# Performance work log

Hardware: AMD Instinct MI355X
Metric: run time of the kernel (lower is better)

Reference implementation:

```python
import jax, jax.numpy as jnp
import numpy as np

DK, DV, NH = 512, 256, 8  # matches init_kwargs


def rel_to_abs(x):
    # x: (B, N, L, 2L-1) -> (B, N, L, L) via pad/reshape trick
    B, N, L, _ = x.shape
    x = jnp.pad(x, ((0, 0), (0, 0), (0, 0), (0, 1)))          # (B,N,L,2L)
    x = x.reshape(B, N, L * 2 * L)
    x = jnp.pad(x, ((0, 0), (0, 0), (0, L - 1)))
    x = x.reshape(B, N, L + 1, 2 * L - 1)
    return x[:, :, :L, L - 1:]


def relative_logits_1d(q, rel_k):
    # q: (B, nh, A, Wd, dkh); rel_k: (dkh, 2*Wd-1)
    B, nh, A, Wd, _ = q.shape
    rel = jnp.einsum('bnawc,cm->bnawm', q, rel_k)             # (B,nh,A,Wd,2Wd-1)
    rel = rel.reshape(B, nh * A, Wd, 2 * Wd - 1)
    rel = rel_to_abs(rel).reshape(B, nh, A, 1, Wd, Wd)
    return jnp.broadcast_to(rel, (B, nh, A, A, Wd, Wd))


def reference(x, w_qkv, w_conv, w_out, key_rel_h, key_rel_w):
    B, Cin, H, W = x.shape
    dkh, dvh = DK // NH, DV // NH
    L = H * W
    # 1x1 qkv projection (stride 1)
    qkv = jnp.einsum('bchw,oc->bohw', x, w_qkv)               # (B, 2dk+dv, H, W)
    q = qkv[:, :DK]
    k = qkv[:, DK:2 * DK]
    v = qkv[:, 2 * DK:]
    flat_q = q.reshape(B, NH, dkh, L) * (dkh ** -0.5)
    flat_k = k.reshape(B, NH, dkh, L)
    flat_v = v.reshape(B, NH, dvh, L)
    logits = jnp.einsum('bncs,bnct->bnst', flat_q, flat_k)     # (B,nh,L,L)
    # relative position logits (uses the already-scaled q, as in the torch code)
    qr = flat_q.reshape(B, NH, dkh, H, W).transpose(0, 1, 3, 4, 2)  # (B,nh,H,W,dkh)
    w_rel = relative_logits_1d(qr, key_rel_w)                  # (B,nh,H,H,W,W)
    h_rel = relative_logits_1d(qr.transpose(0, 1, 3, 2, 4), key_rel_h)  # (B,nh,W,W,H,H)
    h_rel = h_rel.transpose(0, 1, 2, 4, 3, 5).reshape(B, NH, L, L)
    w_rel = w_rel.transpose(0, 1, 4, 2, 5, 3).reshape(B, NH, L, L)
    logits = logits + h_rel + w_rel
    weights = jax.nn.softmax(logits, axis=-1)
    attn = jnp.einsum('bnst,bnct->bnsc', weights, flat_v)      # (B,nh,L,dvh)
    attn = attn.transpose(0, 1, 3, 2).reshape(B, DV, H, W)
    attn = jnp.einsum('bchw,oc->bohw', attn, w_out)            # 1x1 out_proj
    conv_out = jax.lax.conv_general_dilated(
        x, w_conv, window_strides=(1, 1), padding=[(1, 1), (1, 1)],
        dimension_numbers=('NCHW', 'OIHW', 'NCHW'))            # (B, out_c-dv, H, W)
    return jnp.concatenate([conv_out, attn], axis=1)


def setup_inputs() -> dict:
    key = jax.random.key(0)
    ks = jax.random.split(key, 6)
    H, W, Cin = 32, 32, 256
    return {
        'x': jax.random.normal(ks[0], (8, Cin, H, W), jnp.float32),
        'w_qkv': jax.random.normal(ks[1], (2 * DK + DV, Cin), jnp.float32) * 0.02,
        'w_conv': jax.random.normal(ks[2], (256, Cin, 3, 3), jnp.float32) * 0.02,
        'w_out': jax.random.normal(ks[3], (DV, DV), jnp.float32) * 0.02,
        'key_rel_h': DK ** -0.5 + jax.random.normal(ks[4], (DK // NH, 2 * H - 1), jnp.float32),
        'key_rel_w': DK ** -0.5 + jax.random.normal(ks[5], (DK // NH, 2 * W - 1), jnp.float32),
    }
```

## Files before the change

### kernel.cpp

```cpp
#include <hip/hip_runtime.h>
#include <cstddef>
#include <cstdint>

#define NB 8
#define CIN 256
#define LL 1024
#define DKC 512
#define DVC 256
#define XPSTRIDE 295936

typedef short short8 __attribute__((ext_vector_type(8)));
typedef float f32x4 __attribute__((ext_vector_type(4)));

__device__ __forceinline__ unsigned short f2bf(float f) {
  unsigned int u = __float_as_uint(f);
  u += 0x7fffu + ((u >> 16) & 1u);
  return (unsigned short)(u >> 16);
}
__device__ __forceinline__ float bf2f(unsigned short u) {
  return __uint_as_float(((unsigned int)u) << 16);
}

__global__ __launch_bounds__(256) void prep_all(
    const float* __restrict__ x, const float* __restrict__ wconv,
    const float* __restrict__ wqkv, const float* __restrict__ wout,
    const float* __restrict__ krh, const float* __restrict__ krw,
    unsigned short* __restrict__ xTp, unsigned short* __restrict__ wtap,
    unsigned short* __restrict__ wqbf, unsigned short* __restrict__ woutbf,
    unsigned short* __restrict__ relTh, unsigned short* __restrict__ relTw) {
  __shared__ float tile[64][65];
  const int bx = blockIdx.x;
  const int tid = threadIdx.x;
  if (bx < 128) {
    const int st = bx & 15;
    const int b = bx >> 4;
    const int s0 = st * 64;
    const int h0 = st * 2;
    for (int cc = 0; cc < 4; ++cc) {
      const int c0 = cc * 64;
      {
        const int row = tid >> 2;
        const int j0 = (tid & 3) * 16;
#pragma unroll
        for (int k = 0; k < 4; ++k)
          *(float4*)&tile[row][j0 + k * 4] =
              *(const float4*)(x + ((size_t)(b * CIN + c0 + row)) * LL + s0 + j0 + k * 4);
      }
      __syncthreads();
      {
        const int sl = tid >> 2;
        const int cb = (tid & 3) * 16;
        unsigned short buf[16];
#pragma unroll
        for (int m = 0; m < 16; ++m) buf[m] = f2bf(tile[cb + m][sl]);
        const int hp = h0 + (sl >> 5) + 1;
        const int wp = (sl & 31) + 1;
        unsigned short* dst = xTp + (size_t)b * XPSTRIDE + (hp * 34 + wp) * 256 + c0 + cb;
        *(uint4*)dst = *(uint4*)&buf[0];
        *(uint4*)(dst + 8) = *(uint4*)&buf[8];
      }
      __syncthreads();
    }
  } else if (bx < 1184) {
    const int idx = (bx - 128) * 256 + tid;
    const int b = idx / 33792;
    const int rem = idx - b * 33792;
    const int pos = rem >> 8, c = rem & 255;
    int hp, wp;
    if (pos < 34) { hp = 0; wp = pos; }
    else if (pos < 68) { hp = 33; wp = pos - 34; }
    else if (pos < 100) { hp = pos - 68 + 1; wp = 0; }
    else { hp = pos - 100 + 1; wp = 33; }
    xTp[(size_t)b * XPSTRIDE + (hp * 34 + wp) * 256 + c] = 0;
  } else {
    const int idx = (bx - 1184) * 256 + tid;
    if (idx < 589824) {
      const int tap = idx >> 16;
      const int rem = idx & 65535;
      wtap[idx] = f2bf(wconv[(size_t)rem * 9 + tap]);
    } else if (idx < 917504) {
      const int j = idx - 589824;
      const int o = j >> 8;
      const float sc = (o < DKC) ? 0.125f * 1.44269504088896f : 1.0f;
      wqbf[j] = f2bf(wqkv[j] * sc);
    } else if (idx < 983040) {
      const int j = idx - 917504;
      woutbf[j] = f2bf(wout[j]);
    } else {
      const int j = idx - 983040;
      const int tbl = j >> 12;
      const int rest = j & 4095;
      const int m = rest >> 6, c = rest & 63;
      const float* src = tbl ? krw : krh;
      unsigned short* dst = tbl ? relTw : relTh;
      const float v = (m < 63) ? src[c * 63 + m] : 0.f;
      dst[m * 64 + c] = f2bf(v);
    }
  }
}

__global__ __launch_bounds__(256) void qkv_mfma(
    const unsigned short* __restrict__ xTp, const unsigned short* __restrict__ wqbf,
    unsigned short* __restrict__ qbf, unsigned short* __restrict__ kbf,
    unsigned short* __restrict__ vbf) {
  __shared__ __align__(16) char smem[16640];
  unsigned short* as = (unsigned short*)smem;
  unsigned short* bs = (unsigned short*)(smem + 8192);
  float (*trans)[65] = (float(*)[65])smem;

  const int tid = threadIdx.x;
  const int lane = tid & 63, w = tid >> 6;
  const int n16 = lane & 15, quad = lane >> 4;
  const int ot = blockIdx.x;
  const int st = blockIdx.y;
  const int b = blockIdx.z;
  const int o0 = ot * 64;
  const int s0 = st * 64;
  const int h0 = st * 2;
  const int trow = tid >> 3, ck = tid & 7;

  const unsigned short* xb = xTp + (size_t)b * XPSTRIDE;
  const unsigned short* wt = wqbf + (size_t)o0 * 256;
  const int wpos = (trow & 31) + 1;

  f32x4 acc[4];
#pragma unroll
  for (int nt = 0; nt < 4; ++nt) acc[nt] = (f32x4){0.f, 0.f, 0.f, 0.f};

  uint4 ra0, ra1, rb0, rb1;
  {
    ra0 = *(const uint4*)(wt + (size_t)trow * 256 + ck * 8);
    ra1 = *(const uint4*)(wt + (size_t)(trow + 32) * 256 + ck * 8);
    rb0 = *(const uint4*)(xb + (size_t)((h0 + 1) * 34 + wpos) * 256 + ck * 8);
    rb1 = *(const uint4*)(xb + (size_t)((h0 + 2) * 34 + wpos) * 256 + ck * 8);
  }
#pragma unroll
  for (int kc = 0; kc < 4; ++kc) {
    __syncthreads();
    *(uint4*)&as[trow * 64 + ((ck ^ (trow & 7)) * 8)] = ra0;
    *(uint4*)&as[(trow + 32) * 64 + ((ck ^ (trow & 7)) * 8)] = ra1;
    *(uint4*)&bs[trow * 64 + ((ck ^ (trow & 7)) * 8)] = rb0;
    *(uint4*)&bs[(trow + 32) * 64 + ((ck ^ (trow & 7)) * 8)] = rb1;
    __syncthreads();
    if (kc < 3) {
      const int c0 = (kc + 1) * 64;
      ra0 = *(const uint4*)(wt + (size_t)trow * 256 + c0 + ck * 8);
      ra1 = *(const uint4*)(wt + (size_t)(trow + 32) * 256 + c0 + ck * 8);
      rb0 = *(const uint4*)(xb + (size_t)((h0 + 1) * 34 + wpos) * 256 + c0 + ck * 8);
      rb1 = *(const uint4*)(xb + (size_t)((h0 + 2) * 34 + wpos) * 256 + c0 + ck * 8);
    }
    short8 a0 = *(const short8*)&as[(w * 16 + n16) * 64 + ((quad ^ (n16 & 7)) * 8)];
    short8 a1 = *(const short8*)&as[(w * 16 + n16) * 64 + (((quad + 4) ^ (n16 & 7)) * 8)];
#pragma unroll
    for (int nt = 0; nt < 4; ++nt) {
      short8 b0 = *(const short8*)&bs[(nt * 16 + n16) * 64 + ((quad ^ (n16 & 7)) * 8)];
      short8 b1 = *(const short8*)&bs[(nt * 16 + n16) * 64 + (((quad + 4) ^ (n16 & 7)) * 8)];
      acc[nt] = __builtin_amdgcn_mfma_f32_16x16x32_bf16(a0, b0, acc[nt], 0, 0, 0);
      acc[nt] = __builtin_amdgcn_mfma_f32_16x16x32_bf16(a1, b1, acc[nt], 0, 0, 0);
    }
  }
  __syncthreads();
#pragma unroll
  for (int nt = 0; nt < 4; ++nt)
#pragma unroll
    for (int reg = 0; reg < 4; ++reg)
      trans[w * 16 + quad * 4 + reg][nt * 16 + n16] = acc[nt][reg];
  __syncthreads();
  const int sl = tid >> 2;
  const int cseg = (tid & 3) * 16;
  unsigned short buf[16];
  if (ot < 16) {
#pragma unroll
    for (int m = 0; m < 16; ++m) buf[m] = f2bf(trans[cseg + m][sl]);
    unsigned short* dst;
    int head;
    if (ot < 8) { dst = qbf; head = ot; }
    else { dst = kbf; head = ot - 8; }
    const size_t base = (((size_t)(b * 8 + head)) * LL + s0 + sl) * 64 + cseg;
    *(uint4*)(dst + base) = *(uint4*)&buf[0];
    *(uint4*)(dst + base + 8) = *(uint4*)&buf[8];
  } else {
#pragma unroll
    for (int m = 0; m < 16; ++m) buf[m] = f2bf(trans[sl][cseg + m]);
    unsigned short* dst = vbf + ((size_t)b * DVC + (ot - 16) * 64 + sl) * LL + s0 + cseg;
    *(uint4*)dst = *(uint4*)&buf[0];
    *(uint4*)(dst + 8) = *(uint4*)&buf[8];
  }
}

__global__ __launch_bounds__(256, 4) void attn_kernel(
    const unsigned short* __restrict__ qbf, const unsigned short* __restrict__ kbf,
    const unsigned short* __restrict__ vbf, const unsigned short* __restrict__ relTh,
    const unsigned short* __restrict__ relTw, unsigned short* __restrict__ abf) {
  __shared__ __align__(16) char smem[32768];
  unsigned short* ks = (unsigned short*)smem;
  unsigned short* vs = (unsigned short*)(smem + 16384);
  unsigned short* rwtT = (unsigned short*)(smem + 24576);
  unsigned short* ps = (unsigned short*)(smem + 8192);
  float* obuf = (float*)smem;

  const int tid = threadIdx.x;
  const int lane = tid & 63, w = tid >> 6;
  const int n16 = lane & 15, quad = lane >> 4;
  const int blk = blockIdx.x;
  const int bn = blk & 63, qb = blk >> 6;
  const int n = bn & 7, b = bn >> 3;
  const int s0 = qb * 64;
  const int aa = 2 * qb + (w >> 1);
  const int pb = (w & 1) * 16;

  const unsigned short* qbase = qbf + ((size_t)(b * 8 + n)) * LL * 64;
  const unsigned short* kbase = kbf + ((size_t)(b * 8 + n)) * LL * 64;
  const unsigned short* vbase = vbf + ((size_t)(b * 8 + n)) * 32 * LL;

  const int ck = tid & 7;
  const int trow = tid >> 3;
  const int keyt = (trow & 3) | (((trow >> 3) & 1) << 2);
  const int krb = (n16 >> 2) * 8 + (n16 & 3);
  const int kk = (n16 & 3) | (((n16 >> 2) & 1) << 2);
  const int vk = (n16 & 3) | (((n16 >> 3) & 1) << 2);
  const int qcol = w * 16 + n16;

  uint4 pk0 = *(const uint4*)(kbase + trow * 64 + ck * 8);
  uint4 pk1 = *(const uint4*)(kbase + (trow + 32) * 64 + ck * 8);
  uint4 pv = *(const uint4*)(vbase + (size_t)trow * LL + ck * 8);

  {
    const int sT = (pb + n16) * 32 + aa;
    short8 ra0 = *(const short8*)(qbase + (size_t)sT * 64 + quad * 8);
    short8 ra1 = *(const short8*)(qbase + (size_t)sT * 64 + 32 + quad * 8);
#pragma unroll
    for (int tbl = 0; tbl < 2; ++tbl) {
      const unsigned short* rel = tbl ? relTh : relTw;
      f32x4 acc[4];
#pragma unroll
      for (int mt = 0; mt < 4; ++mt) acc[mt] = (f32x4){0.f, 0.f, 0.f, 0.f};
#pragma unroll
      for (int mt = 0; mt < 4; ++mt) {
        short8 b0 = *(const short8*)(rel + (mt * 16 + n16) * 64 + quad * 8);
        short8 b1 = *(const short8*)(rel + (mt * 16 + n16) * 64 + 32 + quad * 8);
        acc[mt] = __builtin_amdgcn_mfma_f32_16x16x32_bf16(ra0, b0, acc[mt], 0, 0, 0);
        acc[mt] = __builtin_amdgcn_mfma_f32_16x16x32_bf16(ra1, b1, acc[mt], 0, 0, 0);
      }
      if (tbl == 0) {
#pragma unroll
        for (int mt = 0; mt < 4; ++mt)
#pragma unroll
          for (int reg = 0; reg < 4; ++reg)
            rwtT[(mt * 16 + n16) * 64 +
                 ((w * 16 + quad * 4 + reg) ^ ((n16 & 7) * 8))] = f2bf(acc[mt][reg]);
      } else {
#pragma unroll
        for (int mt = 0; mt < 4; ++mt)
#pragma unroll
          for (int reg = 0; reg < 4; ++reg)
            ps[(w * 16 + quad * 4 + reg) * 64 + mt * 16 + n16] = f2bf(acc[mt][reg]);
      }
    }
  }
  short8 qf0 = *(const short8*)(qbase + (size_t)(s0 + w * 16 + n16) * 64 + quad * 8);
  short8 qf1 = *(const short8*)(qbase + (size_t)(s0 + w * 16 + n16) * 64 + 32 + quad * 8);
  {
    *(uint4*)&ks[trow * 64 + ((ck ^ keyt) * 8)] = pk0;
    *(uint4*)&ks[(trow + 32) * 64 + ((ck ^ keyt) * 8)] = pk1;
    *(uint4*)&vs[trow * 64 + ((ck ^ keyt) * 8)] = pv;
  }
  __syncthreads();
  float rhreg[2][4];
#pragma unroll
  for (int c1 = 0; c1 < 2; ++c1)
#pragma unroll
    for (int reg = 0; reg < 4; ++reg)
      rhreg[c1][reg] =
          bf2f(ps[qcol * 64 + quad * 8 + c1 * 4 + reg + 31 - pb - n16]);
  __syncthreads();

  float lacc[4] = {0.f, 0.f, 0.f, 0.f};
  f32x4 oacc[2];
  oacc[0] = (f32x4){0.f, 0.f, 0.f, 0.f};
  oacc[1] = (f32x4){0.f, 0.f, 0.f, 0.f};

  int cur = 0;
  for (int kt64 = 0; kt64 < 16; ++kt64) {
    const int t0 = kt64 * 64;
    if (kt64 < 15) {
      const unsigned short* kg = kbase + (size_t)(t0 + 64) * 64;
      pk0 = *(const uint4*)(kg + trow * 64 + ck * 8);
      pk1 = *(const uint4*)(kg + (trow + 32) * 64 + ck * 8);
      pv = *(const uint4*)(vbase + (size_t)trow * LL + t0 + 64 + ck * 8);
    }
    __syncthreads();
    const unsigned short* ksb = ks + cur * 4096;
    const unsigned short* vsb = vs + cur * 2048;

    f32x4 sacc[4];
#pragma unroll
    for (int c = 0; c < 4; ++c) sacc[c] = (f32x4){0.f, 0.f, 0.f, 0.f};
#pragma unroll
    for (int c = 0; c < 4; ++c) {
      const int ro = (krb + (c & 1) * 4 + (c >> 1) * 32) * 64;
      short8 kb0 = *(const short8*)&ksb[ro + ((quad ^ kk) * 8)];
      short8 kb1 = *(const short8*)&ksb[ro + (((quad + 4) ^ kk) * 8)];
      sacc[c] = __builtin_amdgcn_mfma_f32_16x16x32_bf16(kb0, qf0, sacc[c], 0, 0, 0);
      sacc[c] = __builtin_amdgcn_mfma_f32_16x16x32_bf16(kb1, qf1, sacc[c], 0, 0, 0);
    }
    float rww[2];
#pragma unroll
    for (int h = 0; h < 2; ++h) {
      const int mw = (t0 >> 5) + h - aa + 31;
      rww[h] = bf2f(rwtT[mw * 64 + (qcol ^ ((mw & 7) * 8))]);
    }
    unsigned int pkw[2][4];
#pragma unroll
    for (int c = 0; c < 4; ++c) {
      float e[4];
#pragma unroll
      for (int reg = 0; reg < 4; ++reg) {
        e[reg] = __builtin_amdgcn_exp2f(sacc[c][reg] + rww[c >> 1] + rhreg[c & 1][reg]);
        lacc[reg] += e[reg];
      }
      unsigned int p0, p1;
      asm("v_cvt_pk_bf16_f32 %0, %1, %2" : "=v"(p0) : "v"(e[0]), "v"(e[1]));
      asm("v_cvt_pk_bf16_f32 %0, %1, %2" : "=v"(p1) : "v"(e[2]), "v"(e[3]));
      pkw[c >> 1][(c & 1) * 2] = p0;
      pkw[c >> 1][(c & 1) * 2 + 1] = p1;
    }
#pragma unroll
    for (int kt = 0; kt < 2; ++kt) {
      uint4 pw;
      pw.x = pkw[kt][0]; pw.y = pkw[kt][1]; pw.z = pkw[kt][2]; pw.w = pkw[kt][3];
      short8 pa = *(short8*)&pw;
#pragma unroll
      for (int ct = 0; ct < 2; ++ct) {
        short8 vb = *(const short8*)&vsb[(ct * 16 + n16) * 64 + (((quad + 4 * kt) ^ vk) * 8)];
        oacc[ct] = __builtin_amdgcn_mfma_f32_16x16x32_bf16(pa, vb, oacc[ct], 0, 0, 0);
      }
    }
    if (kt64 < 15) {
      unsigned short* kd = ks + (cur ^ 1) * 4096;
      unsigned short* vd = vs + (cur ^ 1) * 2048;
      *(uint4*)&kd[trow * 64 + ((ck ^ keyt) * 8)] = pk0;
      *(uint4*)&kd[(trow + 32) * 64 + ((ck ^ keyt) * 8)] = pk1;
      *(uint4*)&vd[trow * 64 + ((ck ^ keyt) * 8)] = pv;
    }
    cur ^= 1;
  }
  float lsum = (lacc[0] + lacc[1]) + (lacc[2] + lacc[3]);
  lsum += __shfl_xor(lsum, 16);
  lsum += __shfl_xor(lsum, 32);
  const float linv_own = 1.0f / lsum;
  float linv[4];
#pragma unroll
  for (int reg = 0; reg < 4; ++reg)
    linv[reg] = __shfl(linv_own, (lane & 48) | (quad * 4 + reg));
  __syncthreads();
#pragma unroll
  for (int ct = 0; ct < 2; ++ct)
#pragma unroll
    for (int reg = 0; reg < 4; ++reg)
      obuf[(w * 16 + quad * 4 + reg) * 33 + ct * 16 + n16] = oacc[ct][reg] * linv[reg];
  __syncthreads();
  {
    const int row = tid >> 2;
    const int cseg = (tid & 3) * 8;
    unsigned short buf8[8];
#pragma unroll
    for (int m = 0; m < 8; ++m) buf8[m] = f2bf(obuf[row * 33 + cseg + m]);
    *(uint4*)(abf + (((size_t)b * LL) + s0 + row) * 256 + n * 32 + cseg) = *(uint4*)&buf8[0];
  }
}

__global__ __launch_bounds__(256) void convproj_mfma(
    const unsigned short* __restrict__ xTp, const unsigned short* __restrict__ wtap,
    const unsigned short* __restrict__ abf, const unsigned short* __restrict__ woutbf,
    float* __restrict__ out) {
  __shared__ __align__(16) char smem[32768];
  const int tid = threadIdx.x;
  const int lane = tid & 63, w = tid >> 6;
  const int n16 = lane & 15, quad = lane >> 4;
  const int lin = blockIdx.x;
  const int trow = tid >> 3;
  const int ck = tid & 7;

  if (lin < 512) {
    const int ot = lin & 3;
    const int st = (lin >> 2) & 15;
    const int b = lin >> 6;
    const int s0 = st * 64;
    const int h0 = st * 2;
    unsigned short (*as)[64 * 64] = (unsigned short(*)[64 * 64])smem;
    unsigned short (*bs)[64 * 64] = (unsigned short(*)[64 * 64])(smem + 16384);
    const unsigned short* xb = xTp + (size_t)b * XPSTRIDE;
    const unsigned short* wbase = wtap + (size_t)(ot * 64) * 256;

    f32x4 acc[4];
#pragma unroll
    for (int nt = 0; nt < 4; ++nt) acc[nt] = (f32x4){0.f, 0.f, 0.f, 0.f};

    uint4 ra0, ra1, rb0, rb1;
    auto loadtile = [&](int it) {
      const int tap = it >> 2;
      const int c0 = (it & 3) * 64;
      const int dh = tap / 3 - 1;
      const int dw = tap - (tap / 3) * 3 - 1;
      const unsigned short* wt = wbase + (size_t)tap * 65536;
      ra0 = *(const uint4*)(wt + (size_t)trow * 256 + c0 + ck * 8);
      ra1 = *(const uint4*)(wt + (size_t)(trow + 32) * 256 + c0 + ck * 8);
      const int wp = (trow & 31) + dw + 1;
      rb0 = *(const uint4*)(xb + (size_t)((h0 + dh + 1) * 34 + wp) * 256 + c0 + ck * 8);
      rb1 = *(const uint4*)(xb + (size_t)((h0 + dh + 2) * 34 + wp) * 256 + c0 + ck * 8);
    };
    auto stage = [&](int bufi) {
      *(uint4*)&as[bufi][trow * 64 + ((ck ^ (trow & 7)) * 8)] = ra0;
      *(uint4*)&as[bufi][(trow + 32) * 64 + ((ck ^ (trow & 7)) * 8)] = ra1;
      *(uint4*)&bs[bufi][trow * 64 + ((ck ^ (trow & 7)) * 8)] = rb0;
      *(uint4*)&bs[bufi][(trow + 32) * 64 + ((ck ^ (trow & 7)) * 8)] = rb1;
    };
    loadtile(0);
    stage(0);
    for (int it = 0; it < 36; ++it) {
      if (it < 35) loadtile(it + 1);
      __syncthreads();
      const unsigned short* ab = as[it & 1];
      const unsigned short* bb = bs[it & 1];
      short8 a0 = *(const short8*)&ab[(w * 16 + n16) * 64 + ((quad ^ (n16 & 7)) * 8)];
      short8 a1 = *(const short8*)&ab[(w * 16 + n16) * 64 + (((quad + 4) ^ (n16 & 7)) * 8)];
#pragma unroll
      for (int nt = 0; nt < 4; ++nt) {
        short8 b0 = *(const short8*)&bb[(nt * 16 + n16) * 64 + ((quad ^ (n16 & 7)) * 8)];
        short8 b1 = *(const short8*)&bb[(nt * 16 + n16) * 64 + (((quad + 4) ^ (n16 & 7)) * 8)];
        acc[nt] = __builtin_amdgcn_mfma_f32_16x16x32_bf16(a0, b0, acc[nt], 0, 0, 0);
        acc[nt] = __builtin_amdgcn_mfma_f32_16x16x32_bf16(a1, b1, acc[nt], 0, 0, 0);
      }
      if (it < 35) stage((it + 1) & 1);
    }
#pragma unroll
    for (int nt = 0; nt < 4; ++nt)
#pragma unroll
      for (int reg = 0; reg < 4; ++reg)
        out[((size_t)b * 512 + ot * 64 + w * 16 + quad * 4 + reg) * LL + s0 + nt * 16 + n16] =
            acc[nt][reg];
  } else {
    const int l2 = lin - 512;
    const int ot = l2 & 3;
    const int st = (l2 >> 2) & 15;
    const int b = l2 >> 6;
    const int s0 = st * 64;
    const int o0 = ot * 64;
    unsigned short* as = (unsigned short*)smem;
    unsigned short* bs = (unsigned short*)(smem + 16384);
    const unsigned short* ab = abf + ((size_t)b * LL + s0) * 256;
    const unsigned short* wt = woutbf + (size_t)o0 * 256;

    f32x4 acc[4];
#pragma unroll
    for (int nt = 0; nt < 4; ++nt) acc[nt] = (f32x4){0.f, 0.f, 0.f, 0.f};

    uint4 ra0, ra1, rb0, rb1;
    ra0 = *(const uint4*)(wt + (size_t)trow * 256 + ck * 8);
    ra1 = *(const uint4*)(wt + (size_t)(trow + 32) * 256 + ck * 8);
    rb0 = *(const uint4*)(ab + (size_t)trow * 256 + ck * 8);
    rb1 = *(const uint4*)(ab + (size_t)(trow + 32) * 256 + ck * 8);
#pragma unroll
    for (int kc = 0; kc < 4; ++kc) {
      __syncthreads();
      *(uint4*)&as[trow * 64 + ((ck ^ (trow & 7)) * 8)] = ra0;
      *(uint4*)&as[(trow + 32) * 64 + ((ck ^ (trow & 7)) * 8)] = ra1;
      *(uint4*)&bs[trow * 64 + ((ck ^ (trow & 7)) * 8)] = rb0;
      *(uint4*)&bs[(trow + 32) * 64 + ((ck ^ (trow & 7)) * 8)] = rb1;
      __syncthreads();
      if (kc < 3) {
        const int c0 = (kc + 1) * 64;
        ra0 = *(const uint4*)(wt + (size_t)trow * 256 + c0 + ck * 8);
        ra1 = *(const uint4*)(wt + (size_t)(trow + 32) * 256 + c0 + ck * 8);
        rb0 = *(const uint4*)(ab + (size_t)trow * 256 + c0 + ck * 8);
        rb1 = *(const uint4*)(ab + (size_t)(trow + 32) * 256 + c0 + ck * 8);
      }
      short8 a0 = *(const short8*)&as[(w * 16 + n16) * 64 + ((quad ^ (n16 & 7)) * 8)];
      short8 a1 = *(const short8*)&as[(w * 16 + n16) * 64 + (((quad + 4) ^ (n16 & 7)) * 8)];
#pragma unroll
      for (int nt = 0; nt < 4; ++nt) {
        short8 b0 = *(const short8*)&bs[(nt * 16 + n16) * 64 + ((quad ^ (n16 & 7)) * 8)];
        short8 b1 = *(const short8*)&bs[(nt * 16 + n16) * 64 + (((quad + 4) ^ (n16 & 7)) * 8)];
        acc[nt] = __builtin_amdgcn_mfma_f32_16x16x32_bf16(a0, b0, acc[nt], 0, 0, 0);
        acc[nt] = __builtin_amdgcn_mfma_f32_16x16x32_bf16(a1, b1, acc[nt], 0, 0, 0);
      }
    }
#pragma unroll
    for (int nt = 0; nt < 4; ++nt)
#pragma unroll
      for (int reg = 0; reg < 4; ++reg)
        out[((size_t)b * 512 + 256 + o0 + w * 16 + quad * 4 + reg) * LL + s0 + nt * 16 + n16] =
            acc[nt][reg];
  }
}

extern "C" void kernel_launch(void* const* d_in, const int* in_sizes, int n_in,
                              void* d_out, int out_size, void* d_ws, size_t ws_size,
                              hipStream_t stream) {
  const float* x     = (const float*)d_in[0];
  const float* wqkv  = (const float*)d_in[1];
  const float* wconv = (const float*)d_in[2];
  const float* wout  = (const float*)d_in[3];
  const float* krh   = (const float*)d_in[4];
  const float* krw   = (const float*)d_in[5];
  float* out = (float*)d_out;

  unsigned short* qbf = (unsigned short*)d_ws;
  unsigned short* kbf = qbf + (size_t)NB * 8 * LL * 64;
  unsigned short* vbf = kbf + (size_t)NB * 8 * LL * 64;
  unsigned short* abf = vbf + (size_t)NB * DVC * LL;
  unsigned short* relTh = abf + (size_t)NB * LL * DVC;
  unsigned short* relTw = relTh + 4096;
  unsigned short* xTp = relTw + 4096;
  unsigned short* wtap = xTp + (size_t)NB * XPSTRIDE;
  unsigned short* wqbf = wtap + 589824;
  unsigned short* woutbf = wqbf + 327680;

  prep_all<<<dim3(5056), 256, 0, stream>>>(x, wconv, wqkv, wout, krh, krw,
                                           xTp, wtap, wqbf, woutbf, relTh, relTw);
  qkv_mfma<<<dim3(20, 16, NB), 256, 0, stream>>>(xTp, wqbf, qbf, kbf, vbf);
  attn_kernel<<<dim3(1024), 256, 0, stream>>>(qbf, kbf, vbf, relTh, relTw, abf);
  convproj_mfma<<<dim3(1024), 256, 0, stream>>>(xTp, wtap, abf, woutbf, out);
}
```

Baseline: 143.7 us.

## Load K and V fragments directly from global memory instead of LDS staging

Drops the double-buffered LDS staging of K and V tiles in the attention kernel. Each wave now reads its MFMA operand fragments straight from global memory, relying on the L1/L2 caches for reuse across the four waves. This removes the per-iteration block barriers and LDS writes, shrinks shared memory to allow more blocks per CU, and unrolls the key loop by two. In exchange it gives up explicit prefetch, so global-load latency sits directly on the MFMA path, and each K/V element is fetched from cache four times per block.

```diff
diff --git a/kernel.cpp b/kernel.cpp
--- a/kernel.cpp
+++ b/kernel.cpp
@@ -192,13 +192,10 @@
     const unsigned short* __restrict__ qbf, const unsigned short* __restrict__ kbf,
     const unsigned short* __restrict__ vbf, const unsigned short* __restrict__ relTh,
     const unsigned short* __restrict__ relTw, unsigned short* __restrict__ abf) {
-  __shared__ __align__(16) char smem[32768];
-  unsigned short* ks = (unsigned short*)smem;
-  unsigned short* vs = (unsigned short*)(smem + 16384);
-  unsigned short* rwtT = (unsigned short*)(smem + 24576);
-  unsigned short* ps = (unsigned short*)(smem + 8192);
+  __shared__ __align__(16) char smem[16640];
+  unsigned short* ps = (unsigned short*)smem;
+  unsigned short* rwtT = (unsigned short*)(smem + 8192);
   float* obuf = (float*)smem;
-
   const int tid = threadIdx.x;
   const int lane = tid & 63, w = tid >> 6;
   const int n16 = lane & 15, quad = lane >> 4;
@@ -213,17 +210,8 @@
   const unsigned short* kbase = kbf + ((size_t)(b * 8 + n)) * LL * 64;
   const unsigned short* vbase = vbf + ((size_t)(b * 8 + n)) * 32 * LL;
 
-  const int ck = tid & 7;
-  const int trow = tid >> 3;
-  const int keyt = (trow & 3) | (((trow >> 3) & 1) << 2);
   const int krb = (n16 >> 2) * 8 + (n16 & 3);
-  const int kk = (n16 & 3) | (((n16 >> 2) & 1) << 2);
-  const int vk = (n16 & 3) | (((n16 >> 3) & 1) << 2);
   const int qcol = w * 16 + n16;
-
-  uint4 pk0 = *(const uint4*)(kbase + trow * 64 + ck * 8);
-  uint4 pk1 = *(const uint4*)(kbase + (trow + 32) * 64 + ck * 8);
-  uint4 pv = *(const uint4*)(vbase + (size_t)trow * LL + ck * 8);
 
   {
     const int sT = (pb + n16) * 32 + aa;
@@ -260,11 +248,6 @@
   }
   short8 qf0 = *(const short8*)(qbase + (size_t)(s0 + w * 16 + n16) * 64 + quad * 8);
   short8 qf1 = *(const short8*)(qbase + (size_t)(s0 + w * 16 + n16) * 64 + 32 + quad * 8);
-  {
-    *(uint4*)&ks[trow * 64 + ((ck ^ keyt) * 8)] = pk0;
-    *(uint4*)&ks[(trow + 32) * 64 + ((ck ^ keyt) * 8)] = pk1;
-    *(uint4*)&vs[trow * 64 + ((ck ^ keyt) * 8)] = pv;
-  }
   __syncthreads();
   float rhreg[2][4];
 #pragma unroll
@@ -273,34 +256,24 @@
     for (int reg = 0; reg < 4; ++reg)
       rhreg[c1][reg] =
           bf2f(ps[qcol * 64 + quad * 8 + c1 * 4 + reg + 31 - pb - n16]);
-  __syncthreads();
 
   float lacc[4] = {0.f, 0.f, 0.f, 0.f};
   f32x4 oacc[2];
   oacc[0] = (f32x4){0.f, 0.f, 0.f, 0.f};
   oacc[1] = (f32x4){0.f, 0.f, 0.f, 0.f};
 
-  int cur = 0;
+#pragma unroll 2
   for (int kt64 = 0; kt64 < 16; ++kt64) {
     const int t0 = kt64 * 64;
-    if (kt64 < 15) {
-      const unsigned short* kg = kbase + (size_t)(t0 + 64) * 64;
-      pk0 = *(const uint4*)(kg + trow * 64 + ck * 8);
-      pk1 = *(const uint4*)(kg + (trow + 32) * 64 + ck * 8);
-      pv = *(const uint4*)(vbase + (size_t)trow * LL + t0 + 64 + ck * 8);
-    }
-    __syncthreads();
-    const unsigned short* ksb = ks + cur * 4096;
-    const unsigned short* vsb = vs + cur * 2048;
-
     f32x4 sacc[4];
 #pragma unroll
     for (int c = 0; c < 4; ++c) sacc[c] = (f32x4){0.f, 0.f, 0.f, 0.f};
 #pragma unroll
     for (int c = 0; c < 4; ++c) {
-      const int ro = (krb + (c & 1) * 4 + (c >> 1) * 32) * 64;
-      short8 kb0 = *(const short8*)&ksb[ro + ((quad ^ kk) * 8)];
-      short8 kb1 = *(const short8*)&ksb[ro + (((quad + 4) ^ kk) * 8)];
+      const unsigned short* kr =
+          kbase + (size_t)(t0 + krb + (c & 1) * 4 + (c >> 1) * 32) * 64;
+      short8 kb0 = *(const short8*)(kr + quad * 8);
+      short8 kb1 = *(const short8*)(kr + 32 + quad * 8);
       sacc[c] = __builtin_amdgcn_mfma_f32_16x16x32_bf16(kb0, qf0, sacc[c], 0, 0, 0);
       sacc[c] = __builtin_amdgcn_mfma_f32_16x16x32_bf16(kb1, qf1, sacc[c], 0, 0, 0);
     }
@@ -332,18 +305,11 @@
       short8 pa = *(short8*)&pw;
 #pragma unroll
       for (int ct = 0; ct < 2; ++ct) {
-        short8 vb = *(const short8*)&vsb[(ct * 16 + n16) * 64 + (((quad + 4 * kt) ^ vk) * 8)];
+        short8 vb = *(const short8*)(vbase + (size_t)(ct * 16 + n16) * LL + t0 +
+                                     (quad + 4 * kt) * 8);
         oacc[ct] = __builtin_amdgcn_mfma_f32_16x16x32_bf16(pa, vb, oacc[ct], 0, 0, 0);
       }
     }
-    if (kt64 < 15) {
-      unsigned short* kd = ks + (cur ^ 1) * 4096;
-      unsigned short* vd = vs + (cur ^ 1) * 2048;
-      *(uint4*)&kd[trow * 64 + ((ck ^ keyt) * 8)] = pk0;
-      *(uint4*)&kd[(trow + 32) * 64 + ((ck ^ keyt) * 8)] = pk1;
-      *(uint4*)&vd[trow * 64 + ((ck ^ keyt) * 8)] = pv;
-    }
-    cur ^= 1;
   }
   float lsum = (lacc[0] + lacc[1]) + (lacc[2] + lacc[3]);
   lsum += __shfl_xor(lsum, 16);
```

Result: slower. 209.0 us (+45.5%).
